# Optimization experiments

Hardware: AMD Instinct MI355X
Metric: run time of the kernel (lower is better)

## Reference

```python
import jax, jax.numpy as jnp
import numpy as np

VOCAB, EMB, HID = 128000, 128, 1024
B, S = 4, 4096

def setup_inputs() -> dict:
    key = jax.random.key(0)
    k1, k2, k3 = jax.random.split(key, 3)
    x = jax.random.randint(k1, (B, S), 0, VOCAB, dtype=jnp.int64)
    embed_vocab = jax.random.normal(k2, (VOCAB, EMB), dtype=jnp.float32)
    embed_hidden = jax.random.normal(k3, (EMB, HID), dtype=jnp.float32)
    return {"x": x, "embed_vocab": embed_vocab, "embed_hidden": embed_hidden}

def reference(x, embed_vocab, embed_hidden):
    # Faithful to the torch module: build the full factorized table [V,H]
    # then gather rows by token id (F.embedding with defaults: no padding_idx,
    # no max_norm).
    table = embed_vocab @ embed_hidden          # [V, H]
    return jnp.take(table, x, axis=0)           # [B, S, H]
```

## Files before the change

### kernel.cpp

```cpp
#include <hip/hip_runtime.h>


using f32x4 = __attribute__((ext_vector_type(4))) float;
using i32x4 = __attribute__((ext_vector_type(4))) int;
typedef unsigned int u32;

constexpr int EMB = 128;
constexpr int HID = 1024;

__device__ inline void cvt8(const float f[8], i32x4& hi, i32x4& lo) {
    u32 h[8], l[8];
#pragma unroll
    for (int e = 0; e < 8; ++e) {
        u32 fb = __float_as_uint(f[e]);
        u32 hb = fb & 0xFFFF0000u;
        float r = f[e] - __uint_as_float(hb);
        u32 lb = __float_as_uint(r) & 0xFFFF0000u;
        h[e] = hb; l[e] = lb;
    }
#pragma unroll
    for (int p = 0; p < 4; ++p) {
        hi[p] = (int)((h[2*p] >> 16) | h[2*p+1]);
        lo[p] = (int)((l[2*p] >> 16) | l[2*p+1]);
    }
}

__device__ inline f32x4 mfma_bf16(i32x4 a, i32x4 b, f32x4 c) {
    f32x4 d;
    asm volatile("v_mfma_f32_16x16x32_bf16 %0, %1, %2, %3"
                 : "=&v"(d) : "v"(a), "v"(b), "v"(c));
    return d;
}

__global__ __launch_bounds__(256, 2)
void femb(const int* __restrict__ x, const float* __restrict__ ev,
          const float* __restrict__ eh, float* __restrict__ out, int mtiles)
{
    __shared__ __align__(16) u32 lds[2][4][2048];

    const int tid  = threadIdx.x;
    const int lane = tid & 63, wid = tid >> 6;
    const int bid  = blockIdx.x;
    const int mt   = bid % mtiles;
    const int nt   = bid / mtiles;
    const long m0  = (long)mt * 128, n0 = (long)nt * 128;
    const int wm   = wid >> 1, wn = wid & 1;
    const int rl   = lane & 15, g = lane >> 4;

    const int r0 = tid >> 2, aoct = tid & 3;
    const float* abase0 = ev + (long)x[m0 + r0]      * EMB + aoct * 8;
    const float* abase1 = ev + (long)x[m0 + 64 + r0] * EMB + aoct * 8;
    const int bn = tid & 127, boct0 = tid >> 7;
    const float* bcol = eh + n0 + bn;

    float af[2][8], bf[2][8];

    auto loads = [&](int s) {
        const int k0 = s * 32;
#pragma unroll
        for (int h = 0; h < 2; ++h) {
            const float* src = (h ? abase1 : abase0) + k0;
            *(float4*)(&af[h][0]) = *(const float4*)(src);
            *(float4*)(&af[h][4]) = *(const float4*)(src + 4);
        }
#pragma unroll
        for (int h = 0; h < 2; ++h) {
            const int ko = k0 + (boct0 + 2 * h) * 8;
#pragma unroll
            for (int j = 0; j < 8; ++j)
                bf[h][j] = bcol[(long)(ko + j) * HID];
        }
    };

    auto cvtwrite = [&](int buf) {
#pragma unroll
        for (int h = 0; h < 2; ++h) {
            i32x4 hi, lo; cvt8(af[h], hi, lo);
            const int r  = r0 + h * 64;
            const int gs = aoct ^ ((r >> 1) & 3);
            *(i32x4*)&lds[buf][0][r * 16 + gs * 4] = hi;
            *(i32x4*)&lds[buf][1][r * 16 + gs * 4] = lo;
        }
#pragma unroll
        for (int h = 0; h < 2; ++h) {
            i32x4 hi, lo; cvt8(bf[h], hi, lo);
            const int o  = boct0 + 2 * h;
            const int gs = o ^ ((bn >> 1) & 3);
            *(i32x4*)&lds[buf][2][bn * 16 + gs * 4] = hi;
            *(i32x4*)&lds[buf][3][bn * 16 + gs * 4] = lo;
        }
    };

    f32x4 acc[4][4];
#pragma unroll
    for (int i = 0; i < 4; ++i)
#pragma unroll
        for (int j = 0; j < 4; ++j) acc[i][j] = (f32x4){0.f, 0.f, 0.f, 0.f};

    auto compute = [&](int buf) {
        i32x4 bh[4], bl[4];
#pragma unroll
        for (int nf = 0; nf < 4; ++nf) {
            const int nr  = wn * 64 + nf * 16 + rl;
            const int off = nr * 16 + ((g ^ ((nr >> 1) & 3)) << 2);
            bh[nf] = *(const i32x4*)&lds[buf][2][off];
            bl[nf] = *(const i32x4*)&lds[buf][3][off];
        }
#pragma unroll
        for (int mf = 0; mf < 4; ++mf) {
            const int mr  = wm * 64 + mf * 16 + rl;
            const int off = mr * 16 + ((g ^ ((mr >> 1) & 3)) << 2);
            const i32x4 ah = *(const i32x4*)&lds[buf][0][off];
            const i32x4 al = *(const i32x4*)&lds[buf][1][off];
#pragma unroll
            for (int nf = 0; nf < 4; ++nf) {
                acc[mf][nf] = mfma_bf16(ah, bh[nf], acc[mf][nf]);
                acc[mf][nf] = mfma_bf16(ah, bl[nf], acc[mf][nf]);
                acc[mf][nf] = mfma_bf16(al, bh[nf], acc[mf][nf]);
            }
        }
    };

    loads(0);
    cvtwrite(0);
    __builtin_amdgcn_s_waitcnt(0);
    __syncthreads();

#pragma unroll
    for (int s = 0; s < 4; ++s) {
        if (s < 3) loads(s + 1);
        compute(s & 1);
        if (s < 3) cvtwrite((s + 1) & 1);
        __builtin_amdgcn_s_waitcnt(0);
        __syncthreads();
    }

#pragma unroll
    for (int mf = 0; mf < 4; ++mf)
#pragma unroll
        for (int j = 0; j < 4; ++j) {
            const long row = m0 + wm * 64 + mf * 16 + g * 4 + j;
            float* dst = out + row * HID + n0 + wn * 64 + rl;
#pragma unroll
            for (int nf = 0; nf < 4; ++nf) dst[nf * 16] = acc[mf][nf][j];
        }
}

extern "C" void kernel_launch(void* const* d_in, const int* in_sizes, int n_in,
                              void* d_out, int out_size, void* d_ws, size_t ws_size,
                              hipStream_t stream) {
    const int*   x   = (const int*)d_in[0];
    const float* ev  = (const float*)d_in[1];
    const float* eh  = (const float*)d_in[2];
    float*       out = (float*)d_out;

    const int M      = in_sizes[0];
    const int mtiles = M / 128;

    femb<<<mtiles * (HID / 128), 256, 0, stream>>>(x, ev, eh, out, mtiles);
}
```

Baseline: 121.4 us.

## Drop LDS double buffering and register prefetch to raise occupancy

Replaces the double-buffered LDS pipeline, which prefetched the next stage into registers, with a single buffer that loads, converts, writes and then computes each stage in a rolled loop. This halves LDS use to 32 KB and cuts register pressure, so launch bounds can request four blocks per CU instead of two. Separately, the bf16 hi/lo split now packs halves with v_perm instead of shift-and-or. In exchange, the kernel loses overlap of global loads with MFMA work inside a block and relies on other resident blocks to hide that latency.

```diff
diff --git a/kernel.cpp b/kernel.cpp
--- a/kernel.cpp
+++ b/kernel.cpp
@@ -9,19 +9,18 @@
 constexpr int HID = 1024;
 
 __device__ inline void cvt8(const float f[8], i32x4& hi, i32x4& lo) {
-    u32 h[8], l[8];
+    u32 rb[8];
 #pragma unroll
     for (int e = 0; e < 8; ++e) {
         u32 fb = __float_as_uint(f[e]);
-        u32 hb = fb & 0xFFFF0000u;
-        float r = f[e] - __uint_as_float(hb);
-        u32 lb = __float_as_uint(r) & 0xFFFF0000u;
-        h[e] = hb; l[e] = lb;
+        float r = f[e] - __uint_as_float(fb & 0xFFFF0000u);
+        rb[e] = __float_as_uint(r);
     }
 #pragma unroll
     for (int p = 0; p < 4; ++p) {
-        hi[p] = (int)((h[2*p] >> 16) | h[2*p+1]);
-        lo[p] = (int)((l[2*p] >> 16) | l[2*p+1]);
+        hi[p] = (int)__builtin_amdgcn_perm(__float_as_uint(f[2*p+1]),
+                                           __float_as_uint(f[2*p]), 0x07060302u);
+        lo[p] = (int)__builtin_amdgcn_perm(rb[2*p+1], rb[2*p], 0x07060302u);
     }
 }
 
@@ -32,11 +31,11 @@
     return d;
 }
 
-__global__ __launch_bounds__(256, 2)
+__global__ __launch_bounds__(256, 4)
 void femb(const int* __restrict__ x, const float* __restrict__ ev,
           const float* __restrict__ eh, float* __restrict__ out, int mtiles)
 {
-    __shared__ __align__(16) u32 lds[2][4][2048];
+    __shared__ __align__(16) u32 lds[4][2048];
 
     const int tid  = threadIdx.x;
     const int lane = tid & 63, wid = tid >> 6;
@@ -53,65 +52,56 @@
     const int bn = tid & 127, boct0 = tid >> 7;
     const float* bcol = eh + n0 + bn;
 
-    float af[2][8], bf[2][8];
-
-    auto loads = [&](int s) {
-        const int k0 = s * 32;
-#pragma unroll
-        for (int h = 0; h < 2; ++h) {
-            const float* src = (h ? abase1 : abase0) + k0;
-            *(float4*)(&af[h][0]) = *(const float4*)(src);
-            *(float4*)(&af[h][4]) = *(const float4*)(src + 4);
-        }
-#pragma unroll
-        for (int h = 0; h < 2; ++h) {
-            const int ko = k0 + (boct0 + 2 * h) * 8;
-#pragma unroll
-            for (int j = 0; j < 8; ++j)
-                bf[h][j] = bcol[(long)(ko + j) * HID];
-        }
-    };
-
-    auto cvtwrite = [&](int buf) {
-#pragma unroll
-        for (int h = 0; h < 2; ++h) {
-            i32x4 hi, lo; cvt8(af[h], hi, lo);
-            const int r  = r0 + h * 64;
-            const int gs = aoct ^ ((r >> 1) & 3);
-            *(i32x4*)&lds[buf][0][r * 16 + gs * 4] = hi;
-            *(i32x4*)&lds[buf][1][r * 16 + gs * 4] = lo;
-        }
-#pragma unroll
-        for (int h = 0; h < 2; ++h) {
-            i32x4 hi, lo; cvt8(bf[h], hi, lo);
-            const int o  = boct0 + 2 * h;
-            const int gs = o ^ ((bn >> 1) & 3);
-            *(i32x4*)&lds[buf][2][bn * 16 + gs * 4] = hi;
-            *(i32x4*)&lds[buf][3][bn * 16 + gs * 4] = lo;
-        }
-    };
-
     f32x4 acc[4][4];
 #pragma unroll
     for (int i = 0; i < 4; ++i)
 #pragma unroll
         for (int j = 0; j < 4; ++j) acc[i][j] = (f32x4){0.f, 0.f, 0.f, 0.f};
 
-    auto compute = [&](int buf) {
+    auto stagewrite = [&](int s) {
+        const int k0 = s * 32;
+#pragma unroll
+        for (int h = 0; h < 2; ++h) {
+            float f[8];
+            const float* src = (h ? abase1 : abase0) + k0;
+            *(float4*)(&f[0]) = *(const float4*)(src);
+            *(float4*)(&f[4]) = *(const float4*)(src + 4);
+            i32x4 hi, lo; cvt8(f, hi, lo);
+            const int r  = r0 + h * 64;
+            const int gs = aoct ^ ((r >> 1) & 3);
+            *(i32x4*)&lds[0][r * 16 + gs * 4] = hi;
+            *(i32x4*)&lds[1][r * 16 + gs * 4] = lo;
+        }
+#pragma unroll
+        for (int h = 0; h < 2; ++h) {
+            const int o  = boct0 + 2 * h;
+            const int ko = k0 + o * 8;
+            float f[8];
+#pragma unroll
+            for (int j = 0; j < 8; ++j)
+                f[j] = bcol[(long)(ko + j) * HID];
+            i32x4 hi, lo; cvt8(f, hi, lo);
+            const int gs = o ^ ((bn >> 1) & 3);
+            *(i32x4*)&lds[2][bn * 16 + gs * 4] = hi;
+            *(i32x4*)&lds[3][bn * 16 + gs * 4] = lo;
+        }
+    };
+
+    auto compute = [&]() {
         i32x4 bh[4], bl[4];
 #pragma unroll
         for (int nf = 0; nf < 4; ++nf) {
             const int nr  = wn * 64 + nf * 16 + rl;
             const int off = nr * 16 + ((g ^ ((nr >> 1) & 3)) << 2);
-            bh[nf] = *(const i32x4*)&lds[buf][2][off];
-            bl[nf] = *(const i32x4*)&lds[buf][3][off];
+            bh[nf] = *(const i32x4*)&lds[2][off];
+            bl[nf] = *(const i32x4*)&lds[3][off];
         }
 #pragma unroll
         for (int mf = 0; mf < 4; ++mf) {
             const int mr  = wm * 64 + mf * 16 + rl;
             const int off = mr * 16 + ((g ^ ((mr >> 1) & 3)) << 2);
-            const i32x4 ah = *(const i32x4*)&lds[buf][0][off];
-            const i32x4 al = *(const i32x4*)&lds[buf][1][off];
+            const i32x4 ah = *(const i32x4*)&lds[0][off];
+            const i32x4 al = *(const i32x4*)&lds[1][off];
 #pragma unroll
             for (int nf = 0; nf < 4; ++nf) {
                 acc[mf][nf] = mfma_bf16(ah, bh[nf], acc[mf][nf]);
@@ -121,18 +111,13 @@
         }
     };
 
-    loads(0);
-    cvtwrite(0);
-    __builtin_amdgcn_s_waitcnt(0);
-    __syncthreads();
-
-#pragma unroll
+#pragma unroll 1
     for (int s = 0; s < 4; ++s) {
-        if (s < 3) loads(s + 1);
-        compute(s & 1);
-        if (s < 3) cvtwrite((s + 1) & 1);
+        if (s) __syncthreads();
+        stagewrite(s);
         __builtin_amdgcn_s_waitcnt(0);
         __syncthreads();
+        compute();
     }
 
 #pragma unroll
```

Measured after the change: 120.5 us. Within noise of the previous version (-0.7%).
